# Optimization experiments

Hardware: AMD Instinct MI355X
Metric: run time of the kernel (lower is better)

## Reference

```python
import jax, jax.numpy as jnp
import numpy as np

HIDDEN = 2048
N_HEADS = 16
N_KV_HEADS = 4
HEAD_DIM = HIDDEN // N_HEADS  # 128
ROPE_THETA = 10000.0
BATCH = 2
SEQ = 2048


def setup_inputs() -> dict:
    key = jax.random.key(0)
    k1, k2, k3, k4, k5 = jax.random.split(key, 5)
    s = 0.02
    return {
        "hidden_states": jax.random.normal(k1, (BATCH, SEQ, HIDDEN), dtype=jnp.float32),
        "attention_mask": jnp.zeros((BATCH, 1, 1, SEQ), dtype=jnp.float32),
        "Wq": jax.random.normal(k2, (HIDDEN, N_HEADS * HEAD_DIM), dtype=jnp.float32) * s,
        "Wk": jax.random.normal(k3, (HIDDEN, N_KV_HEADS * HEAD_DIM), dtype=jnp.float32) * s,
        "Wv": jax.random.normal(k4, (HIDDEN, N_KV_HEADS * HEAD_DIM), dtype=jnp.float32) * s,
        "Wo": jax.random.normal(k5, (N_HEADS * HEAD_DIM, HIDDEN), dtype=jnp.float32) * s,
    }


def _rope_cos_sin(seq_len, dtype):
    inv_freq = 1.0 / (ROPE_THETA ** (jnp.arange(0, HEAD_DIM, 2, dtype=jnp.float32) / HEAD_DIM))
    t = jnp.arange(seq_len, dtype=jnp.float32)
    freqs = t[:, None] * inv_freq[None, :]            # [S, D/2]
    emb = jnp.concatenate([freqs, freqs], axis=-1)    # [S, D]
    cos = jnp.cos(emb)[None, None, :, :].astype(dtype)  # [1,1,S,D]
    sin = jnp.sin(emb)[None, None, :, :].astype(dtype)
    return cos, sin


def _apply_rope(x, cos, sin):
    # x: [B,H,S,D]; faithful to torch code: rotated = cat((-x[...,1::2], x[...,::2]), -1)
    x1 = x[..., ::2]
    x2 = x[..., 1::2]
    rotated = jnp.concatenate([-x2, x1], axis=-1)
    return x * cos + rotated * sin


def reference(hidden_states, attention_mask, Wq, Wk, Wv, Wo):
    B, S, _ = hidden_states.shape
    scale = HEAD_DIM ** -0.5

    q = (hidden_states @ Wq).reshape(B, S, N_HEADS, HEAD_DIM).transpose(0, 2, 1, 3)      # [B,H,S,D]
    k = (hidden_states @ Wk).reshape(B, S, N_KV_HEADS, HEAD_DIM).transpose(0, 2, 1, 3)   # [B,KV,S,D]
    v = (hidden_states @ Wv).reshape(B, S, N_KV_HEADS, HEAD_DIM).transpose(0, 2, 1, 3)

    cos, sin = _rope_cos_sin(S, hidden_states.dtype)
    q = _apply_rope(q, cos, sin)
    k = _apply_rope(k, cos, sin)

    rep = N_HEADS // N_KV_HEADS
    k = jnp.repeat(k, rep, axis=1)  # [B,H,S,D]
    v = jnp.repeat(v, rep, axis=1)

    scores = jnp.einsum("bhqd,bhkd->bhqk", q, k) * scale  # [B,H,S,S]
    causal = jnp.tril(jnp.ones((S, S), dtype=bool))[None, None]
    scores = jnp.where(causal, scores, -jnp.inf)
    scores = scores + attention_mask  # additive float mask, broadcast [B,1,1,S]

    attn = jax.nn.softmax(scores, axis=-1)
    out = jnp.einsum("bhqk,bhkd->bhqd", attn, v)           # [B,H,S,D]
    out = out.transpose(0, 2, 1, 3).reshape(B, S, N_HEADS * HEAD_DIM)
    return out @ Wo
```

## Files before the change

### kernel.cpp

```cpp
#include <hip/hip_runtime.h>
#include <hip/hip_bf16.h>

#define BATCH 2
#define SEQ   2048
#define NH    16
#define NKV   4
#define HD    128
#define KDIM  2048
#define MROWS 4096
#define NQKV  3072

typedef __attribute__((ext_vector_type(8))) short  s16x8;
typedef __attribute__((ext_vector_type(4))) short  s16x4;
typedef __attribute__((ext_vector_type(4))) float  f32x4;
typedef __attribute__((ext_vector_type(8))) __bf16 b16x8;

#define BARRIER_LDS() do { \
    asm volatile("s_waitcnt lgkmcnt(0)" ::: "memory"); \
    __builtin_amdgcn_s_barrier(); \
  } while (0)

__device__ __forceinline__ unsigned short f2bf(float f) {
  __hip_bfloat16 h = __float2bfloat16(f);
  return *reinterpret_cast<unsigned short*>(&h);
}
__device__ __forceinline__ float bf2f(unsigned short h) {
  union { unsigned int u; float f; } x; x.u = ((unsigned int)h) << 16;
  return x.f;
}

__device__ __forceinline__ f32x4 MFMA16(s16x8 a, s16x8 b, f32x4 c) {
  return __builtin_amdgcn_mfma_f32_16x16x32_bf16(
      __builtin_bit_cast(b16x8, a), __builtin_bit_cast(b16x8, b), c, 0, 0, 0);
}

__device__ __forceinline__ void gload_lds16(const void* g, void* lds) {
  __builtin_amdgcn_global_load_lds(
      (const __attribute__((address_space(1))) void*)g,
      (__attribute__((address_space(3))) void*)lds, 16, 0, 0);
}

__global__ __launch_bounds__(256) void prep_weights(
    const float* __restrict__ Wq, const float* __restrict__ Wk,
    const float* __restrict__ Wv, const float* __restrict__ Wo,
    unsigned short* __restrict__ BT, unsigned short* __restrict__ WoT) {
  __shared__ float tile[32][33];
  int bx = blockIdx.x;
  const float* W; unsigned short* WT; int Nd, nb;
  if (bx < 64)       { W = Wq; WT = BT;                          Nd = 2048; nb = bx; }
  else if (bx < 80)  { W = Wk; WT = BT + (size_t)2048 * KDIM;    Nd = 512;  nb = bx - 64; }
  else if (bx < 96)  { W = Wv; WT = BT + (size_t)2560 * KDIM;    Nd = 512;  nb = bx - 80; }
  else               { W = Wo; WT = WoT;                         Nd = 2048; nb = bx - 96; }
  int n0 = nb * 32, k0 = blockIdx.y * 32;
  int tx = threadIdx.x & 31, ty = threadIdx.x >> 5;
#pragma unroll
  for (int i = 0; i < 4; ++i)
    tile[ty + i * 8][tx] = W[(size_t)(k0 + ty + i * 8) * Nd + n0 + tx];
  __syncthreads();
#pragma unroll
  for (int i = 0; i < 4; ++i)
    WT[(size_t)(n0 + ty + i * 8) * KDIM + k0 + tx] = f2bf(tile[tx][ty + i * 8]);
}

__global__ __launch_bounds__(256) void conv_bf16(
    const float* __restrict__ X, unsigned short* __restrict__ Y) {
  int i = blockIdx.x * 256 + threadIdx.x;
  const float4 a = ((const float4*)X)[2 * i];
  const float4 b = ((const float4*)X)[2 * i + 1];
  s16x8 o;
  o[0] = (short)f2bf(a.x); o[1] = (short)f2bf(a.y);
  o[2] = (short)f2bf(a.z); o[3] = (short)f2bf(a.w);
  o[4] = (short)f2bf(b.x); o[5] = (short)f2bf(b.y);
  o[6] = (short)f2bf(b.z); o[7] = (short)f2bf(b.w);
  ((s16x8*)Y)[i] = o;
}

__global__ __launch_bounds__(256) void rope_table_kernel(float* __restrict__ tbl) {
  int i = blockIdx.x * 256 + threadIdx.x;
  int s = i >> 6, j = i & 63;
  float inv = powf(10000.0f, -(float)(2 * j) * (1.0f / 128.0f));
  float f = (float)s * inv;
  tbl[2 * i]     = cosf(f);
  tbl[2 * i + 1] = sinf(f);
}

__global__ __launch_bounds__(512, 2) void gemm_qkv(
    const unsigned short* __restrict__ A, const unsigned short* __restrict__ BT,
    unsigned short* __restrict__ Qo, unsigned short* __restrict__ Ko,
    unsigned short* __restrict__ Vo) {
  __shared__ __align__(16) unsigned short lds[4][2][8192];
  int tid = threadIdx.x, lane = tid & 63;
  int w = tid >> 6, wm = w >> 2, wn = w & 3;
  int lin = blockIdx.x;
  int swz = (lin & 7) * 24 + (lin >> 3);
  int bx = swz % 12, by = swz / 12;
  int m0 = by * 256, n0 = bx * 256;
  int fr = lane & 15, cg4 = lane >> 4, rg4 = (lane >> 4) * 4;

  int rS1 = tid >> 2,        cS1 = (tid & 3) ^ (rS1 & 3);
  int t2  = tid + 512;
  int rS2 = t2 >> 2,         cS2 = (t2 & 3) ^ (rS2 & 3);

  f32x4 acc[8][4] = {};

#pragma unroll
  for (int kt = 0; kt < 2; ++kt) {
    gload_lds16(A + (size_t)(m0 + rS1) * KDIM + kt * 32 + cS1 * 8,
                (char*)&lds[kt][0][0] + (size_t)tid * 16);
    gload_lds16(A + (size_t)(m0 + rS2) * KDIM + kt * 32 + cS2 * 8,
                (char*)&lds[kt][0][0] + (size_t)t2 * 16);
    gload_lds16(BT + (size_t)(n0 + rS1) * KDIM + kt * 32 + cS1 * 8,
                (char*)&lds[kt][1][0] + (size_t)tid * 16);
    gload_lds16(BT + (size_t)(n0 + rS2) * KDIM + kt * 32 + cS2 * 8,
                (char*)&lds[kt][1][0] + (size_t)t2 * 16);
  }

  for (int kt = 0; kt < KDIM / 32; ++kt) {
    int buf = kt & 3;
    asm volatile("s_waitcnt vmcnt(4)" ::: "memory");
    __builtin_amdgcn_s_barrier();

    const unsigned short* lA = &lds[buf][0][0];
    const unsigned short* lB = &lds[buf][1][0];
    s16x8 bfr[4], afr[4];
#pragma unroll
    for (int nf = 0; nf < 4; ++nf) {
      int rb = wn * 64 + nf * 16 + fr;
      bfr[nf] = *(const s16x8*)(lB + rb * 32 + (cg4 ^ (rb & 3)) * 8);
    }
#pragma unroll
    for (int mf = 0; mf < 4; ++mf) {
      int ra = wm * 128 + mf * 16 + fr;
      afr[mf] = *(const s16x8*)(lA + ra * 32 + (cg4 ^ (ra & 3)) * 8);
    }
    if (kt + 2 < KDIM / 32) {
      int nb = (kt + 2) & 3, ko = (kt + 2) * 32;
      gload_lds16(A + (size_t)(m0 + rS1) * KDIM + ko + cS1 * 8,
                  (char*)&lds[nb][0][0] + (size_t)tid * 16);
      gload_lds16(A + (size_t)(m0 + rS2) * KDIM + ko + cS2 * 8,
                  (char*)&lds[nb][0][0] + (size_t)t2 * 16);
    }
    __builtin_amdgcn_s_setprio(1);
#pragma unroll
    for (int mf = 0; mf < 4; ++mf)
#pragma unroll
      for (int nf = 0; nf < 4; ++nf)
        acc[mf][nf] = MFMA16(afr[mf], bfr[nf], acc[mf][nf]);
    __builtin_amdgcn_s_setprio(0);
#pragma unroll
    for (int mf = 0; mf < 4; ++mf) {
      int ra = wm * 128 + (mf + 4) * 16 + fr;
      afr[mf] = *(const s16x8*)(lA + ra * 32 + (cg4 ^ (ra & 3)) * 8);
    }
    if (kt + 2 < KDIM / 32) {
      int nb = (kt + 2) & 3, ko = (kt + 2) * 32;
      gload_lds16(BT + (size_t)(n0 + rS1) * KDIM + ko + cS1 * 8,
                  (char*)&lds[nb][1][0] + (size_t)tid * 16);
      gload_lds16(BT + (size_t)(n0 + rS2) * KDIM + ko + cS2 * 8,
                  (char*)&lds[nb][1][0] + (size_t)t2 * 16);
    }
    __builtin_amdgcn_s_setprio(1);
#pragma unroll
    for (int mf = 0; mf < 4; ++mf)
#pragma unroll
      for (int nf = 0; nf < 4; ++nf)
        acc[mf + 4][nf] = MFMA16(afr[mf], bfr[nf], acc[mf + 4][nf]);
    __builtin_amdgcn_s_setprio(0);
  }

  int rbase = m0 + wm * 128 + rg4;
#pragma unroll
  for (int nf = 0; nf < 4; ++nf) {
    int gn = n0 + wn * 64 + nf * 16 + fr;
    if (gn < 2048) {
      int hh = gn >> 7, d = gn & 127;
#pragma unroll
      for (int mf = 0; mf < 8; ++mf)
#pragma unroll
        for (int r = 0; r < 4; ++r) {
          int grow = rbase + mf * 16 + r;
          int bb = grow >> 11, ss = grow & 2047;
          Qo[((size_t)(bb * NH + hh) * SEQ + ss) * HD + d] = f2bf(acc[mf][nf][r]);
        }
    } else if (gn < 2560) {
      int c = gn - 2048, kvh = c >> 7, d = c & 127;
#pragma unroll
      for (int mf = 0; mf < 8; ++mf)
#pragma unroll
        for (int r = 0; r < 4; ++r) {
          int grow = rbase + mf * 16 + r;
          int bb = grow >> 11, ss = grow & 2047;
          Ko[((size_t)(bb * NKV + kvh) * SEQ + ss) * HD + d] = f2bf(acc[mf][nf][r]);
        }
    } else {
      int c = gn - 2560, kvh = c >> 7, d = c & 127;
#pragma unroll
      for (int mf = 0; mf < 8; ++mf) {
        int grow0 = rbase + mf * 16;
        int bb = grow0 >> 11, ss = grow0 & 2047;
        s16x4 pk;
#pragma unroll
        for (int r = 0; r < 4; ++r) pk[r] = (short)f2bf(acc[mf][nf][r]);
        *(s16x4*)(Vo + ((size_t)(bb * NKV + kvh) * HD + d) * SEQ + ss) = pk;
      }
    }
  }
}

__global__ __launch_bounds__(256) void gemm_out(
    const unsigned short* __restrict__ A, const unsigned short* __restrict__ BT,
    float* __restrict__ C) {
  __shared__ __align__(16) unsigned short la[128][32];
  __shared__ __align__(16) unsigned short lb[128][32];
  int tid = threadIdx.x, lane = tid & 63, w = tid >> 6;
  int lin = blockIdx.x;
  int swz = (lin & 7) * 64 + (lin >> 3);
  int bx = swz % 16, by = swz / 16;
  int m0 = by * 128, n0 = bx * 128;
  int wr = (w >> 1) * 64, wc = (w & 1) * 64;
  int fr = lane & 15, kg = (lane >> 4) * 8, rg = (lane >> 4) * 4;
  f32x4 acc[4][4] = {};
  for (int kt = 0; kt < KDIM; kt += 32) {
    __syncthreads();
#pragma unroll
    for (int i = 0; i < 2; ++i) {
      int idx = tid + i * 256;
      int row = idx >> 2, seg = idx & 3;
      gload_lds16(A + (size_t)(m0 + row) * KDIM + kt + seg * 8,
                  (char*)la + (size_t)(i * 256 + w * 64) * 16);
      gload_lds16(BT + (size_t)(n0 + row) * KDIM + kt + seg * 8,
                  (char*)lb + (size_t)(i * 256 + w * 64) * 16);
    }
    __syncthreads();
    s16x8 af[4], bf[4];
#pragma unroll
    for (int mi = 0; mi < 4; ++mi) af[mi] = *(const s16x8*)(&la[wr + mi * 16 + fr][kg]);
#pragma unroll
    for (int ni = 0; ni < 4; ++ni) bf[ni] = *(const s16x8*)(&lb[wc + ni * 16 + fr][kg]);
#pragma unroll
    for (int mi = 0; mi < 4; ++mi)
#pragma unroll
      for (int ni = 0; ni < 4; ++ni) acc[mi][ni] = MFMA16(af[mi], bf[ni], acc[mi][ni]);
  }
  int rbase = m0 + wr + rg;
#pragma unroll
  for (int ni = 0; ni < 4; ++ni) {
    int gn = n0 + wc + ni * 16 + fr;
#pragma unroll
    for (int mi = 0; mi < 4; ++mi)
#pragma unroll
      for (int r = 0; r < 4; ++r)
        C[(size_t)(rbase + mi * 16 + r) * 2048 + gn] = acc[mi][ni][r];
  }
}

__global__ __launch_bounds__(256) void rope2(
    unsigned short* __restrict__ Qx, unsigned short* __restrict__ Kx,
    const float* __restrict__ tbl) {
  __shared__ __align__(16) unsigned short xs[32][136];
  int tid = threadIdx.x;
  int bid = blockIdx.x;
  unsigned short* X;
  size_t r0;
  if (bid < 2048) { X = Qx; r0 = (size_t)bid * 32; }
  else            { X = Kx; r0 = (size_t)(bid - 2048) * 32; }
#pragma unroll
  for (int i = 0; i < 2; ++i) {
    int idx = tid + i * 256;
    int pr = idx >> 4, seg = idx & 15;
    *(s16x8*)(&xs[pr][seg * 8]) = *(const s16x8*)(X + (r0 + pr) * 128 + seg * 8);
  }
  __syncthreads();
  int pr = tid >> 3, jb = (tid & 7) * 8;
  size_t row = r0 + pr;
  int s = (int)(row & (SEQ - 1));
  s16x8 o0, o1;
#pragma unroll
  for (int j0 = 0; j0 < 8; ++j0) {
    int j = jb + j0;
    float c  = tbl[(s * 64 + j) * 2];
    float sn = tbl[(s * 64 + j) * 2 + 1];
    float xj   = bf2f(xs[pr][j]);
    float xj64 = bf2f(xs[pr][j + 64]);
    float x2j  = bf2f(xs[pr][2 * j]);
    float x2j1 = bf2f(xs[pr][2 * j + 1]);
    o0[j0] = (short)f2bf(xj * c - x2j1 * sn);
    o1[j0] = (short)f2bf(xj64 * c + x2j * sn);
  }
  unsigned short* xp = X + row * 128;
  *(s16x8*)(xp + jb)      = o0;
  *(s16x8*)(xp + 64 + jb) = o1;
}

__global__ __launch_bounds__(256, 2) void attn_fwd(
    const unsigned short* __restrict__ Q, const unsigned short* __restrict__ K,
    const unsigned short* __restrict__ VT, const float* __restrict__ mask,
    unsigned short* __restrict__ O) {
  __shared__ __align__(16) unsigned short kt_[2][64][136];
  __shared__ __align__(16) unsigned short vt_[2][128][68];
  __shared__ __align__(16) unsigned short pt_[4][16][36];

  int tid = threadIdx.x, lane = tid & 63, w = tid >> 6;
  int l = blockIdx.x;
  int grp = l & 7, slot = l >> 3;
  int hloc = slot & 3, qt = 31 - (slot >> 2);
  int b = grp >> 2, kvh = grp & 3, h = kvh * 4 + hloc;
  int qbase = qt * 64;
  int qw = qbase + w * 16;
  int fr = lane & 15, g = lane >> 4, kg = g * 8, rg = g * 4;

  const unsigned short* Qb = Q + (size_t)(b * NH + h) * SEQ * HD;
  const unsigned short* Kb = K + (size_t)(b * NKV + kvh) * SEQ * HD;
  const unsigned short* Vb = VT + (size_t)(b * NKV + kvh) * HD * SEQ;
  const float* mb = mask + (size_t)b * SEQ;

  int krow = tid >> 4, kpos = (tid & 15) * 8;
  const float sc2 = 0.12751744584812722f;
  const float L2E = 1.44269504088896f;
  int bS = b * SEQ;
  int ntiles = qt + 1;

  s16x8 aq[4];
#pragma unroll
  for (int dc = 0; dc < 4; ++dc)
    aq[dc] = *(const s16x8*)(Qb + (size_t)(qw + fr) * HD + dc * 32 + kg);

  f32x4 oacc[8] = {};
  float m_r = -3e38f, l_r = 0.f;

  s16x8 kreg[4], vreg[4];
#pragma unroll
  for (int i = 0; i < 4; ++i)
    kreg[i] = *(const s16x8*)(Kb + (size_t)(krow + i * 16) * HD + kpos);
#pragma unroll
  for (int i = 0; i < 4; ++i) {
    int c = tid + 256 * i;
    vreg[i] = *(const s16x8*)(Vb + (size_t)(c >> 3) * SEQ + (c & 7) * 8);
  }
#pragma unroll
  for (int i = 0; i < 4; ++i)
    *(s16x8*)(&kt_[0][krow + i * 16][kpos]) = kreg[i];
#pragma unroll
  for (int i = 0; i < 4; ++i) {
    int c = tid + 256 * i;
    *(s16x8*)(&vt_[0][c >> 3][(c & 7) * 8]) = vreg[i];
  }
  if (ntiles > 1) {
#pragma unroll
    for (int i = 0; i < 4; ++i)
      kreg[i] = *(const s16x8*)(Kb + (size_t)(64 + krow + i * 16) * HD + kpos);
#pragma unroll
    for (int i = 0; i < 4; ++i) {
      int c = tid + 256 * i;
      vreg[i] = *(const s16x8*)(Vb + (size_t)(c >> 3) * SEQ + 64 + (c & 7) * 8);
    }
  }
  BARRIER_LDS();

  for (int t = 0; t < ntiles; ++t) {
    int kv0 = t * 64;
    int cur = t & 1;
    bool diag = (t == qt);

    if (t + 1 < ntiles) {
#pragma unroll
      for (int i = 0; i < 4; ++i)
        *(s16x8*)(&kt_[cur ^ 1][krow + i * 16][kpos]) = kreg[i];
#pragma unroll
      for (int i = 0; i < 4; ++i) {
        int c = tid + 256 * i;
        *(s16x8*)(&vt_[cur ^ 1][c >> 3][(c & 7) * 8]) = vreg[i];
      }
      if (t + 2 < ntiles) {
#pragma unroll
        for (int i = 0; i < 4; ++i)
          kreg[i] = *(const s16x8*)(Kb + (size_t)(kv0 + 128 + krow + i * 16) * HD + kpos);
#pragma unroll
        for (int i = 0; i < 4; ++i) {
          int c = tid + 256 * i;
          vreg[i] = *(const s16x8*)(Vb + (size_t)(c >> 3) * SEQ + kv0 + 128 + (c & 7) * 8);
        }
      }
    }

    f32x4 sf[4];
    __builtin_amdgcn_s_setprio(1);
#pragma unroll
    for (int mk = 0; mk < 4; ++mk) {
      s16x8 ak[4];
#pragma unroll
      for (int dc = 0; dc < 4; ++dc)
        ak[dc] = *(const s16x8*)(&kt_[cur][mk * 16 + fr][dc * 32 + kg]);
      sf[mk] = f32x4{0.f, 0.f, 0.f, 0.f};
#pragma unroll
      for (int dc = 0; dc < 4; ++dc)
        sf[mk] = MFMA16(ak[dc], aq[dc], sf[mk]);
    }
    __builtin_amdgcn_s_setprio(0);

#pragma unroll
    for (int mk = 0; mk < 4; ++mk) {
      float4 mv = *(const float4*)(mb + kv0 + mk * 16 + rg);
      float mvr[4] = {mv.x * L2E, mv.y * L2E, mv.z * L2E, mv.w * L2E};
      if (diag) {
#pragma unroll
        for (int r = 0; r < 4; ++r) {
          int kv = kv0 + mk * 16 + rg + r;
          float v = sf[mk][r] * sc2 + mvr[r];
          sf[mk][r] = (kv <= qw + fr) ? v : -3e38f;
        }
      } else {
#pragma unroll
        for (int r = 0; r < 4; ++r)
          sf[mk][r] = sf[mk][r] * sc2 + mvr[r];
      }
    }

    float pm01a = fmaxf(sf[0][0], sf[0][1]), pm01b = fmaxf(sf[0][2], sf[0][3]);
    float pm11a = fmaxf(sf[1][0], sf[1][1]), pm11b = fmaxf(sf[1][2], sf[1][3]);
    float pm21a = fmaxf(sf[2][0], sf[2][1]), pm21b = fmaxf(sf[2][2], sf[2][3]);
    float pm31a = fmaxf(sf[3][0], sf[3][1]), pm31b = fmaxf(sf[3][2], sf[3][3]);
    float pm0 = fmaxf(pm01a, pm01b), pm1 = fmaxf(pm11a, pm11b);
    float pm2 = fmaxf(pm21a, pm21b), pm3 = fmaxf(pm31a, pm31b);
    float pm = fmaxf(fmaxf(pm0, pm1), fmaxf(pm2, pm3));
    pm = fmaxf(pm, __shfl_xor(pm, 16, 64));
    pm = fmaxf(pm, __shfl_xor(pm, 32, 64));
    if (!__all(pm - m_r <= 8.0f)) {
      float mo = m_r;
      float mn = fmaxf(mo, pm);
      float al = exp2f(mo - mn);
      m_r = mn;
      l_r *= al;
#pragma unroll
      for (int r = 0; r < 4; ++r) {
        float ar = __shfl(al, rg + r, 16);
#pragma unroll
        for (int od = 0; od < 8; ++od) oacc[od][r] *= ar;
      }
    }
    float rs = 0.f;
#pragma unroll
    for (int mk = 0; mk < 4; ++mk)
#pragma unroll
      for (int r = 0; r < 4; ++r) {
        float ppv = exp2f(sf[mk][r] - m_r);
        sf[mk][r] = ppv;
        rs += ppv;
      }
    rs += __shfl_xor(rs, 16, 64);
    rs += __shfl_xor(rs, 32, 64);
    l_r += rs;

#pragma unroll
    for (int kk = 0; kk < 2; ++kk) {
#pragma unroll
      for (int mh = 0; mh < 2; ++mh) {
        int mk = kk * 2 + mh;
        s16x4 pk;
#pragma unroll
        for (int r = 0; r < 4; ++r) pk[r] = (short)f2bf(sf[mk][r]);
        *(s16x4*)(&pt_[w][fr][mh * 16 + rg]) = pk;
      }
      s16x8 ap = *(const s16x8*)(&pt_[w][fr][kg]);
      __builtin_amdgcn_s_setprio(1);
#pragma unroll
      for (int od = 0; od < 8; ++od) {
        s16x8 bv = *(const s16x8*)(&vt_[cur][od * 16 + fr][kk * 32 + kg]);
        oacc[od] = MFMA16(ap, bv, oacc[od]);
      }
      __builtin_amdgcn_s_setprio(0);
    }

    BARRIER_LDS();
  }

  float iv = 1.0f / l_r;
  float ivr[4];
#pragma unroll
  for (int r = 0; r < 4; ++r) ivr[r] = __shfl(iv, rg + r, 16);
#pragma unroll
  for (int r = 0; r < 4; ++r) {
    unsigned short* op = O + (size_t)(bS + qw + rg + r) * 2048 + h * 128 + fr;
#pragma unroll
    for (int od = 0; od < 8; ++od)
      op[od * 16] = f2bf(oacc[od][r] * ivr[r]);
  }
}

extern "C" void kernel_launch(void* const* d_in, const int* in_sizes, int n_in,
                              void* d_out, int out_size, void* d_ws, size_t ws_size,
                              hipStream_t stream) {
  const float* hidden = (const float*)d_in[0];
  const float* mask   = (const float*)d_in[1];
  const float* Wq     = (const float*)d_in[2];
  const float* Wk     = (const float*)d_in[3];
  const float* Wv     = (const float*)d_in[4];
  const float* Wo     = (const float*)d_in[5];
  float* out = (float*)d_out;

  char* ws = (char*)d_ws;
  unsigned short* BT  = (unsigned short*)(ws);
  unsigned short* WoT = (unsigned short*)(ws + 12582912);
  unsigned short* Qb  = (unsigned short*)(ws + 20971520);
  unsigned short* Kb  = (unsigned short*)(ws + 37748736);
  unsigned short* VT  = (unsigned short*)(ws + 41943040);
  unsigned short* AO  = (unsigned short*)(ws + 46137344);
  float*          tbl = (float*)(ws + 62914560);
  unsigned short* Ab  = AO;

  conv_bf16<<<MROWS * KDIM / (256 * 8), 256, 0, stream>>>(hidden, Ab);
  prep_weights<<<dim3(160, 64), 256, 0, stream>>>(Wq, Wk, Wv, Wo, BT, WoT);
  rope_table_kernel<<<512, 256, 0, stream>>>(tbl);

  gemm_qkv<<<dim3(192), 512, 0, stream>>>(Ab, BT, Qb, Kb, VT);
  rope2<<<dim3(2048 + 512), 256, 0, stream>>>(Qb, Kb, tbl);
  attn_fwd<<<dim3(1024), 256, 0, stream>>>(Qb, Kb, VT, mask, AO);
  gemm_out<<<dim3(512), 256, 0, stream>>>(AO, WoT, out);
}
```

Baseline: 223.0 us.

## Rewrite output projection GEMM with 256x128 tiles and 4-stage pipelined LDS loads

```diff
diff --git a/kernel.cpp b/kernel.cpp
--- a/kernel.cpp
+++ b/kernel.cpp
@@ -207,50 +207,97 @@
   }
 }
 
-__global__ __launch_bounds__(256) void gemm_out(
+__global__ __launch_bounds__(512, 1) void gemm_out(
     const unsigned short* __restrict__ A, const unsigned short* __restrict__ BT,
     float* __restrict__ C) {
-  __shared__ __align__(16) unsigned short la[128][32];
-  __shared__ __align__(16) unsigned short lb[128][32];
-  int tid = threadIdx.x, lane = tid & 63, w = tid >> 6;
+  __shared__ __align__(16) unsigned short ldsA[4][8192];
+  __shared__ __align__(16) unsigned short ldsB[4][4096];
+  int tid = threadIdx.x, lane = tid & 63;
+  int w = tid >> 6, wm = w >> 2, wn = w & 3;
   int lin = blockIdx.x;
-  int swz = (lin & 7) * 64 + (lin >> 3);
+  int swz = (lin & 7) * 32 + (lin >> 3);
   int bx = swz % 16, by = swz / 16;
-  int m0 = by * 128, n0 = bx * 128;
-  int wr = (w >> 1) * 64, wc = (w & 1) * 64;
-  int fr = lane & 15, kg = (lane >> 4) * 8, rg = (lane >> 4) * 4;
-  f32x4 acc[4][4] = {};
-  for (int kt = 0; kt < KDIM; kt += 32) {
-    __syncthreads();
-#pragma unroll
-    for (int i = 0; i < 2; ++i) {
-      int idx = tid + i * 256;
-      int row = idx >> 2, seg = idx & 3;
-      gload_lds16(A + (size_t)(m0 + row) * KDIM + kt + seg * 8,
-                  (char*)la + (size_t)(i * 256 + w * 64) * 16);
-      gload_lds16(BT + (size_t)(n0 + row) * KDIM + kt + seg * 8,
-                  (char*)lb + (size_t)(i * 256 + w * 64) * 16);
-    }
-    __syncthreads();
-    s16x8 af[4], bf[4];
-#pragma unroll
-    for (int mi = 0; mi < 4; ++mi) af[mi] = *(const s16x8*)(&la[wr + mi * 16 + fr][kg]);
-#pragma unroll
-    for (int ni = 0; ni < 4; ++ni) bf[ni] = *(const s16x8*)(&lb[wc + ni * 16 + fr][kg]);
-#pragma unroll
-    for (int mi = 0; mi < 4; ++mi)
-#pragma unroll
-      for (int ni = 0; ni < 4; ++ni) acc[mi][ni] = MFMA16(af[mi], bf[ni], acc[mi][ni]);
-  }
-  int rbase = m0 + wr + rg;
-#pragma unroll
-  for (int ni = 0; ni < 4; ++ni) {
-    int gn = n0 + wc + ni * 16 + fr;
-#pragma unroll
-    for (int mi = 0; mi < 4; ++mi)
+  int m0 = by * 256, n0 = bx * 128;
+  int fr = lane & 15, cg4 = lane >> 4, rg4 = (lane >> 4) * 4;
+
+  int rS1 = tid >> 2,  cS1 = (tid & 3) ^ (rS1 & 3);
+  int t2  = tid + 512;
+  int rS2 = t2 >> 2,   cS2 = (t2 & 3) ^ (rS2 & 3);
+  int rB  = tid >> 2,  cB  = (tid & 3) ^ (rB & 3);
+  bool doB = (tid < 512);
+
+  f32x4 acc[8][2] = {};
+
+#pragma unroll
+  for (int kt = 0; kt < 2; ++kt) {
+    gload_lds16(A + (size_t)(m0 + rS1) * KDIM + kt * 32 + cS1 * 8,
+                (char*)&ldsA[kt][0] + (size_t)tid * 16);
+    gload_lds16(A + (size_t)(m0 + rS2) * KDIM + kt * 32 + cS2 * 8,
+                (char*)&ldsA[kt][0] + (size_t)t2 * 16);
+    gload_lds16(BT + (size_t)(n0 + rB) * KDIM + kt * 32 + cB * 8,
+                (char*)&ldsB[kt][0] + (size_t)tid * 16);
+  }
+
+  for (int kt = 0; kt < KDIM / 32; ++kt) {
+    int buf = kt & 3;
+    asm volatile("s_waitcnt vmcnt(3)" ::: "memory");
+    __builtin_amdgcn_s_barrier();
+
+    const unsigned short* lA = &ldsA[buf][0];
+    const unsigned short* lB = &ldsB[buf][0];
+    s16x8 bfr[2], afr[4];
+#pragma unroll
+    for (int nf = 0; nf < 2; ++nf) {
+      int rb = wn * 32 + nf * 16 + fr;
+      bfr[nf] = *(const s16x8*)(lB + rb * 32 + (cg4 ^ (rb & 3)) * 8);
+    }
+#pragma unroll
+    for (int mf = 0; mf < 4; ++mf) {
+      int ra = wm * 128 + mf * 16 + fr;
+      afr[mf] = *(const s16x8*)(lA + ra * 32 + (cg4 ^ (ra & 3)) * 8);
+    }
+    if (kt + 2 < KDIM / 32) {
+      int nb = (kt + 2) & 3, ko = (kt + 2) * 32;
+      gload_lds16(A + (size_t)(m0 + rS1) * KDIM + ko + cS1 * 8,
+                  (char*)&ldsA[nb][0] + (size_t)tid * 16);
+      gload_lds16(A + (size_t)(m0 + rS2) * KDIM + ko + cS2 * 8,
+                  (char*)&ldsA[nb][0] + (size_t)t2 * 16);
+    }
+    __builtin_amdgcn_s_setprio(1);
+#pragma unroll
+    for (int mf = 0; mf < 4; ++mf)
+#pragma unroll
+      for (int nf = 0; nf < 2; ++nf)
+        acc[mf][nf] = MFMA16(afr[mf], bfr[nf], acc[mf][nf]);
+    __builtin_amdgcn_s_setprio(0);
+#pragma unroll
+    for (int mf = 0; mf < 4; ++mf) {
+      int ra = wm * 128 + (mf + 4) * 16 + fr;
+      afr[mf] = *(const s16x8*)(lA + ra * 32 + (cg4 ^ (ra & 3)) * 8);
+    }
+    if (kt + 2 < KDIM / 32) {
+      int nb = (kt + 2) & 3, ko = (kt + 2) * 32;
+      gload_lds16(BT + (size_t)(n0 + rB) * KDIM + ko + cB * 8,
+                  (char*)&ldsB[nb][0] + (size_t)tid * 16);
+    }
+    __builtin_amdgcn_s_setprio(1);
+#pragma unroll
+    for (int mf = 0; mf < 4; ++mf)
+#pragma unroll
+      for (int nf = 0; nf < 2; ++nf)
+        acc[mf + 4][nf] = MFMA16(afr[mf], bfr[nf], acc[mf + 4][nf]);
+    __builtin_amdgcn_s_setprio(0);
+  }
+
+  int rbase = m0 + wm * 128 + rg4;
+#pragma unroll
+  for (int nf = 0; nf < 2; ++nf) {
+    int gn = n0 + wn * 32 + nf * 16 + fr;
+#pragma unroll
+    for (int mf = 0; mf < 8; ++mf)
 #pragma unroll
       for (int r = 0; r < 4; ++r)
-        C[(size_t)(rbase + mi * 16 + r) * 2048 + gn] = acc[mi][ni][r];
+        C[(size_t)(rbase + mf * 16 + r) * 2048 + gn] = acc[mf][nf][r];
   }
 }
 
@@ -515,5 +562,5 @@
   gemm_qkv<<<dim3(192), 512, 0, stream>>>(Ab, BT, Qb, Kb, VT);
   rope2<<<dim3(2048 + 512), 256, 0, stream>>>(Qb, Kb, tbl);
   attn_fwd<<<dim3(1024), 256, 0, stream>>>(Qb, Kb, VT, mask, AO);
-  gemm_out<<<dim3(512), 256, 0, stream>>>(AO, WoT, out);
-}
+  gemm_out<<<dim3(256), 512, 0, stream>>>(AO, WoT, out);
+}
```

Result: no change. 220.5 us (-1.1%).
